# Performance work log

Measured on AMD Instinct MI355X. Metric: run time of the kernel, lower is better.

## Reference

```python
import math
import jax, jax.numpy as jnp
import numpy as np

B, N, C = 2, 2048, 256
TOPK_COARSE = 128
TOPK_FINE = 16
LOCAL_RAD = math.radians(15.0)
TEMP = 0.07
NEG = -1e9


def setup_inputs() -> dict:
    key = jax.random.key(0)
    ks = jax.random.split(key, 8)
    feat_a = jax.random.normal(ks[0], (B, N, C), jnp.float32)
    feat_b = jax.random.normal(ks[1], (B, N, C), jnp.float32)
    da = jax.random.normal(ks[2], (B, N, 3), jnp.float32)
    db = jax.random.normal(ks[3], (B, N, 3), jnp.float32)
    dirs_a = da / jnp.linalg.norm(da, axis=-1, keepdims=True)
    dirs_b = db / jnp.linalg.norm(db, axis=-1, keepdims=True)
    s = 1.0 / np.sqrt(C).astype(np.float32)
    Wq = jax.random.normal(ks[4], (C, C), jnp.float32) * s
    bq = jax.random.normal(ks[5], (C,), jnp.float32) * 0.01
    Wk = jax.random.normal(ks[6], (C, C), jnp.float32) * s
    bk = jax.random.normal(ks[7], (C,), jnp.float32) * 0.01
    return {"feat_a": feat_a, "feat_b": feat_b, "dirs_a": dirs_a, "dirs_b": dirs_b,
            "Wq": Wq, "bq": bq, "Wk": Wk, "bk": bk}


def reference(feat_a, feat_b, dirs_a, dirs_b, Wq, bq, Wk, bk):
    b, n, c = feat_a.shape
    q = feat_a @ Wq.T + bq                         # [B,N,C]
    k = feat_b @ Wk.T + bk                         # [B,N,C]

    # coarse stage: top-k over full similarity (math identical to chunked topk)
    sim = jnp.einsum('bnc,bmc->bnm', q, k)         # [B,N,N]
    _, coarse_idx = jax.lax.top_k(sim, TOPK_COARSE)  # [B,N,Kc]

    bi = jnp.arange(b)[:, None, None]
    k_cand = k[bi, coarse_idx]                     # [B,N,Kc,C]
    db_cand = dirs_b[bi, coarse_idx]               # [B,N,Kc,3]

    # angular locality mask (non-differentiable path)
    cosang = jnp.clip(jnp.sum(dirs_a[:, :, None, :] * db_cand, -1), -1.0, 1.0)
    ang = jnp.arccos(jax.lax.stop_gradient(cosang))
    local_mask = ang <= LOCAL_RAD                  # [B,N,Kc]
    # per-row fallback to all-ones (subsumes the chunk-level torch.any check)
    valid = local_mask.any(-1, keepdims=True)
    eff = jnp.where(valid, local_mask, True)

    logits_full = jnp.einsum('bnc,bnkc->bnk', q, k_cand) / TEMP
    logits_full = jnp.where(eff, logits_full, NEG)

    # fine stage: keep top TOPK_FINE candidates per row
    topk_vals, topk_pos = jax.lax.top_k(logits_full, TOPK_FINE)  # [B,N,Kf]
    idx = jnp.take_along_axis(coarse_idx, topk_pos, -1)
    eff_f = jnp.take_along_axis(eff, topk_pos, -1)
    fallback = eff_f.any(-1, keepdims=True)
    eff_f = jnp.where(fallback, eff_f, True)
    logits = jnp.where(eff_f, topk_vals, NEG)

    probs = jax.nn.softmax(logits, axis=-1) * eff_f.astype(logits.dtype)

    # scatter sparse support into dense P (indices distinct per row -> set is safe)
    ri = jnp.arange(n)[None, :, None]
    P = jnp.zeros((b, n, n), feat_a.dtype).at[bi, ri, idx].set(probs)
    P = P / (P.sum(-1, keepdims=True) + 1e-8)
    return P
```

## Files before the change

### kernel.cpp

```cpp
#include <hip/hip_runtime.h>
#include <hip/hip_bf16.h>
#include <math.h>

#define NN_ 2048
#define CC_ 256
#define KC_ 128
#define KF_ 16
#define EQCAP 64

typedef __attribute__((ext_vector_type(8))) short short8;
typedef __attribute__((ext_vector_type(4))) float f32x4;

__device__ __forceinline__ unsigned int mono_u(float f) {
  unsigned int u = __float_as_uint(f);
  return (u & 0x80000000u) ? ~u : (u | 0x80000000u);
}
__device__ __forceinline__ float inv_mono(unsigned int m) {
  unsigned int u = (m & 0x80000000u) ? (m ^ 0x80000000u) : ~m;
  return __uint_as_float(u);
}

__device__ __forceinline__ void gload_lds16(const void* g, void* l) {
  __builtin_amdgcn_global_load_lds(
      (const __attribute__((address_space(1))) void*)g,
      (__attribute__((address_space(3))) void*)l, 16, 0, 0);
}

__device__ __forceinline__ unsigned short bf16_bits(float v) {
  __hip_bfloat16 h = __float2bfloat16(v);
  return *(unsigned short*)&h;
}
__device__ __forceinline__ float bf16_val(unsigned short u) {
  __hip_bfloat16 h = *(__hip_bfloat16*)&u;
  return __bfloat162float(h);
}

__global__ __launch_bounds__(256) void proj_mfma_kernel(
    const float* __restrict__ fa, const float* __restrict__ fb,
    const float* __restrict__ Wq, const float* __restrict__ bq,
    const float* __restrict__ Wk, const float* __restrict__ bk,
    __hip_bfloat16* __restrict__ qh, __hip_bfloat16* __restrict__ ql,
    __hip_bfloat16* __restrict__ kh, __hip_bfloat16* __restrict__ kl)
{
  __shared__ short Ah[64 * 32], Al[64 * 32], Bh[64 * 32], Bl[64 * 32];
  const int m0 = blockIdx.y * 64;
  const int z = m0 >> 12;
  const int mloc = m0 & 4095;
  const float* A = z ? fb : fa;
  const float* W = z ? Wk : Wq;
  const float* bias = z ? bk : bq;
  __hip_bfloat16* oh = z ? kh : qh;
  __hip_bfloat16* ol = z ? kl : ql;
  const int n0 = blockIdx.x * 64;
  const int tid = threadIdx.x;
  const int lane = tid & 63, wave = tid >> 6;
  const int wm = (wave & 1) << 5, wn = (wave >> 1) << 5;
  const int fm = lane & 15, quad = lane >> 4;

  const int r = tid >> 3;
  const int r2 = r + 32;
  const int c4 = (tid & 7) << 2;
  const int ck = c4 >> 3;
  const int soff = c4 & 7;
  const int iA0 = (((r << 2) + (ck ^ ((r >> 1) & 3))) << 3) + soff;
  const int iA1 = (((r2 << 2) + (ck ^ ((r2 >> 1) & 3))) << 3) + soff;

  f32x4 acc[2][2];
#pragma unroll
  for (int i = 0; i < 2; ++i)
#pragma unroll
    for (int j = 0; j < 2; ++j) acc[i][j] = (f32x4){0.f, 0.f, 0.f, 0.f};

  for (int kb = 0; kb < CC_; kb += 32) {
    float4 va0 = *(const float4*)(A + (long)(mloc + r) * CC_ + kb + c4);
    float4 va1 = *(const float4*)(A + (long)(mloc + r2) * CC_ + kb + c4);
    float4 vb0 = *(const float4*)(W + (long)(n0 + r) * CC_ + kb + c4);
    float4 vb1 = *(const float4*)(W + (long)(n0 + r2) * CC_ + kb + c4);
    __syncthreads();
    {
      const float* pv;
      float4 vv;
      vv = va0; pv = (const float*)&vv;
      uint2 hu, lu;
      unsigned short h0 = bf16_bits(pv[0]), h1 = bf16_bits(pv[1]),
                     h2 = bf16_bits(pv[2]), h3 = bf16_bits(pv[3]);
      hu.x = (unsigned)h0 | ((unsigned)h1 << 16);
      hu.y = (unsigned)h2 | ((unsigned)h3 << 16);
      lu.x = (unsigned)bf16_bits(pv[0] - bf16_val(h0)) |
             ((unsigned)bf16_bits(pv[1] - bf16_val(h1)) << 16);
      lu.y = (unsigned)bf16_bits(pv[2] - bf16_val(h2)) |
             ((unsigned)bf16_bits(pv[3] - bf16_val(h3)) << 16);
      *(uint2*)&Ah[iA0] = hu; *(uint2*)&Al[iA0] = lu;
      vv = va1; pv = (const float*)&vv;
      h0 = bf16_bits(pv[0]); h1 = bf16_bits(pv[1]);
      h2 = bf16_bits(pv[2]); h3 = bf16_bits(pv[3]);
      hu.x = (unsigned)h0 | ((unsigned)h1 << 16);
      hu.y = (unsigned)h2 | ((unsigned)h3 << 16);
      lu.x = (unsigned)bf16_bits(pv[0] - bf16_val(h0)) |
             ((unsigned)bf16_bits(pv[1] - bf16_val(h1)) << 16);
      lu.y = (unsigned)bf16_bits(pv[2] - bf16_val(h2)) |
             ((unsigned)bf16_bits(pv[3] - bf16_val(h3)) << 16);
      *(uint2*)&Ah[iA1] = hu; *(uint2*)&Al[iA1] = lu;
      vv = vb0; pv = (const float*)&vv;
      h0 = bf16_bits(pv[0]); h1 = bf16_bits(pv[1]);
      h2 = bf16_bits(pv[2]); h3 = bf16_bits(pv[3]);
      hu.x = (unsigned)h0 | ((unsigned)h1 << 16);
      hu.y = (unsigned)h2 | ((unsigned)h3 << 16);
      lu.x = (unsigned)bf16_bits(pv[0] - bf16_val(h0)) |
             ((unsigned)bf16_bits(pv[1] - bf16_val(h1)) << 16);
      lu.y = (unsigned)bf16_bits(pv[2] - bf16_val(h2)) |
             ((unsigned)bf16_bits(pv[3] - bf16_val(h3)) << 16);
      *(uint2*)&Bh[iA0] = hu; *(uint2*)&Bl[iA0] = lu;
      vv = vb1; pv = (const float*)&vv;
      h0 = bf16_bits(pv[0]); h1 = bf16_bits(pv[1]);
      h2 = bf16_bits(pv[2]); h3 = bf16_bits(pv[3]);
      hu.x = (unsigned)h0 | ((unsigned)h1 << 16);
      hu.y = (unsigned)h2 | ((unsigned)h3 << 16);
      lu.x = (unsigned)bf16_bits(pv[0] - bf16_val(h0)) |
             ((unsigned)bf16_bits(pv[1] - bf16_val(h1)) << 16);
      lu.y = (unsigned)bf16_bits(pv[2] - bf16_val(h2)) |
             ((unsigned)bf16_bits(pv[3] - bf16_val(h3)) << 16);
      *(uint2*)&Bh[iA1] = hu; *(uint2*)&Bl[iA1] = lu;
    }
    __syncthreads();
    short8 afh[2], afl[2], bfh[2], bfl[2];
#pragma unroll
    for (int t = 0; t < 2; ++t) {
      int m = wm + (t << 4) + fm;
      int sa = ((m << 2) + (quad ^ ((m >> 1) & 3))) << 3;
      afh[t] = *(const short8*)&Ah[sa];
      afl[t] = *(const short8*)&Al[sa];
      int n = wn + (t << 4) + fm;
      int sb = ((n << 2) + (quad ^ ((n >> 1) & 3))) << 3;
      bfh[t] = *(const short8*)&Bh[sb];
      bfl[t] = *(const short8*)&Bl[sb];
    }
#pragma unroll
    for (int mi = 0; mi < 2; ++mi)
#pragma unroll
      for (int ni = 0; ni < 2; ++ni) {
        acc[mi][ni] = __builtin_amdgcn_mfma_f32_16x16x32_bf16(
            afh[mi], bfh[ni], acc[mi][ni], 0, 0, 0);
        acc[mi][ni] = __builtin_amdgcn_mfma_f32_16x16x32_bf16(
            afh[mi], bfl[ni], acc[mi][ni], 0, 0, 0);
        acc[mi][ni] = __builtin_amdgcn_mfma_f32_16x16x32_bf16(
            afl[mi], bfh[ni], acc[mi][ni], 0, 0, 0);
      }
  }

#pragma unroll
  for (int mi = 0; mi < 2; ++mi)
#pragma unroll
    for (int ni = 0; ni < 2; ++ni) {
      int nn = n0 + wn + (ni << 4) + fm;
      float bval = bias[nn];
      int mrow = mloc + wm + (mi << 4) + (quad << 2);
#pragma unroll
      for (int reg = 0; reg < 4; ++reg) {
        float v = acc[mi][ni][reg] + bval;
        __hip_bfloat16 h = __float2bfloat16(v);
        long idx = (long)(mrow + reg) * CC_ + nn;
        oh[idx] = h;
        ol[idx] = __float2bfloat16(v - __bfloat162float(h));
      }
    }
}

__global__ __launch_bounds__(256) void sim_mfma_kernel(
    const __hip_bfloat16* __restrict__ qh, const __hip_bfloat16* __restrict__ ql,
    const __hip_bfloat16* __restrict__ kh, const __hip_bfloat16* __restrict__ kl,
    float* __restrict__ sim)
{
  __shared__ short Ah[128 * 32], Al[128 * 32], Bh[128 * 32], Bl[128 * 32];
  const int z = blockIdx.z;
  const long off = (long)z * NN_ * CC_;
  const int m0 = blockIdx.y * 128, n0 = blockIdx.x * 128;
  const int tid = threadIdx.x;
  const int lane = tid & 63, wave = tid >> 6;
  const int wm = (wave & 1) << 6, wn = (wave >> 1) << 6;
  const int fm = lane & 15, quad = lane >> 4;

  const int r0 = tid >> 2, r1 = r0 + 64;
  const int c0 = (((tid & 3) ^ ((r0 >> 1) & 3)) << 3);
  const int c1 = (((tid & 3) ^ ((r1 >> 1) & 3)) << 3);
  const long lo0 = (long)tid * 8, lo1 = ((long)tid + 256) * 8;
  const long gA0 = (long)(m0 + r0) * CC_ + c0 + off;
  const long gA1 = (long)(m0 + r1) * CC_ + c1 + off;
  const long gB0 = (long)(n0 + r0) * CC_ + c0 + off;
  const long gB1 = (long)(n0 + r1) * CC_ + c1 + off;

  f32x4 acc[4][4];
#pragma unroll
  for (int i = 0; i < 4; ++i)
#pragma unroll
    for (int j = 0; j < 4; ++j) acc[i][j] = (f32x4){0.f, 0.f, 0.f, 0.f};

  for (int kb = 0; kb < CC_; kb += 32) {
    gload_lds16(qh + gA0 + kb, Ah + lo0);
    gload_lds16(qh + gA1 + kb, Ah + lo1);
    gload_lds16(ql + gA0 + kb, Al + lo0);
    gload_lds16(ql + gA1 + kb, Al + lo1);
    gload_lds16(kh + gB0 + kb, Bh + lo0);
    gload_lds16(kh + gB1 + kb, Bh + lo1);
    gload_lds16(kl + gB0 + kb, Bl + lo0);
    gload_lds16(kl + gB1 + kb, Bl + lo1);
    __syncthreads();
    short8 afh[4], afl[4], bfh[4], bfl[4];
#pragma unroll
    for (int t = 0; t < 4; ++t) {
      int m = wm + (t << 4) + fm;
      int sa = ((m << 2) + (quad ^ ((m >> 1) & 3))) << 3;
      afh[t] = *(const short8*)&Ah[sa];
      afl[t] = *(const short8*)&Al[sa];
      int n = wn + (t << 4) + fm;
      int sb = ((n << 2) + (quad ^ ((n >> 1) & 3))) << 3;
      bfh[t] = *(const short8*)&Bh[sb];
      bfl[t] = *(const short8*)&Bl[sb];
    }
#pragma unroll
    for (int mi = 0; mi < 4; ++mi)
#pragma unroll
      for (int ni = 0; ni < 4; ++ni) {
        acc[mi][ni] = __builtin_amdgcn_mfma_f32_16x16x32_bf16(
            afh[mi], bfh[ni], acc[mi][ni], 0, 0, 0);
        acc[mi][ni] = __builtin_amdgcn_mfma_f32_16x16x32_bf16(
            afh[mi], bfl[ni], acc[mi][ni], 0, 0, 0);
        acc[mi][ni] = __builtin_amdgcn_mfma_f32_16x16x32_bf16(
            afl[mi], bfh[ni], acc[mi][ni], 0, 0, 0);
      }
    __syncthreads();
  }

  float* Cp = sim + (long)z * NN_ * NN_;
#pragma unroll
  for (int mi = 0; mi < 4; ++mi) {
#pragma unroll
    for (int ni = 0; ni < 4; ++ni) {
      int m = m0 + wm + (mi << 4) + (quad << 2);
      int n = n0 + wn + (ni << 4) + fm;
      float* p = Cp + (long)m * NN_ + n;
      p[0] = acc[mi][ni][0];
      p[NN_] = acc[mi][ni][1];
      p[2 * NN_] = acc[mi][ni][2];
      p[3 * NN_] = acc[mi][ni][3];
    }
  }
}

__global__ __launch_bounds__(256) void select_scatter_kernel(
    const float* __restrict__ sim, const float* __restrict__ dirs_a,
    const float* __restrict__ dirs_b, float* __restrict__ P)
{
  const int wave = threadIdx.x >> 6;
  const int lane = threadIdx.x & 63;
  const int row = (blockIdx.x << 2) | wave;
  const int b = row >> 11;
  const float* srow = sim + (long)row * NN_;
  float* prow = P + (long)row * NN_;

  __shared__ unsigned int ckey_s[4][KC_];
  __shared__ int cidx_s[4][KC_];
  __shared__ int eq_s[4][EQCAP];
  __shared__ float outp_s[4][KF_];
  __shared__ int outj_s[4][KF_];
  __shared__ float rowbuf_s[4][1024];
  __shared__ int cnt_s[4][2];

  unsigned int* ckey = ckey_s[wave];
  int* cidx = cidx_s[wave];
  int* eqb = eq_s[wave];
  float* outp = outp_s[wave];
  int* outj = outj_s[wave];
  float* rowbuf = rowbuf_s[wave];
  int* cnt = cnt_s[wave];

  unsigned int key[32];
#pragma unroll
  for (int c = 0; c < 8; ++c) {
    float4 v = *(const float4*)(srow + (c << 8) + (lane << 2));
    key[(c << 2) + 0] = mono_u(v.x);
    key[(c << 2) + 1] = mono_u(v.y);
    key[(c << 2) + 2] = mono_u(v.z);
    key[(c << 2) + 3] = mono_u(v.w);
  }

  unsigned int lo = 0u, hi = 0xFFFFFFFFu;
  while (hi - lo > 1u) {
    unsigned int mid = lo + ((hi - lo) >> 1);
    int c = 0;
#pragma unroll
    for (int i = 0; i < 32; ++i)
      c += __popcll(__ballot(key[i] >= mid));
    if (c >= KC_) lo = mid; else hi = mid;
  }
  const unsigned int T = lo;
  int cgt = 0;
#pragma unroll
  for (int i = 0; i < 32; ++i)
    cgt += __popcll(__ballot(key[i] > T));
  const int count_gt = cgt;
  const int need_eq = KC_ - cgt;

  if (lane == 0) { cnt[0] = 0; cnt[1] = 0; }
#pragma unroll
  for (int i = 0; i < 32; ++i) {
    unsigned int u = key[i];
    int col = ((i >> 2) << 8) + (lane << 2) + (i & 3);
    if (u > T) {
      int p = atomicAdd(&cnt[0], 1);
      ckey[p] = u;
      cidx[p] = col;
    } else if (u == T) {
      int p = atomicAdd(&cnt[1], 1);
      if (p < EQCAP) eqb[p] = col;
    }
  }
  int neq = cnt[1];
  if (lane == 0) {
    if (neq <= EQCAP) {
      for (int r = 0; r < need_eq; ++r) {
        int best = 0x7FFFFFFF, bi = 0;
        for (int t2 = 0; t2 < neq; ++t2)
          if (eqb[t2] < best) { best = eqb[t2]; bi = t2; }
        eqb[bi] = 0x7FFFFFFF;
        ckey[count_gt + r] = T;
        cidx[count_gt + r] = best;
      }
    } else {
      int r2 = 0;
      for (int j = 0; j < NN_ && r2 < need_eq; ++j)
        if (mono_u(srow[j]) == T) {
          ckey[count_gt + r2] = T;
          cidx[count_gt + r2] = j;
          ++r2;
        }
    }
  }

  const long dbase = (long)row * 3;
  const float dax = dirs_a[dbase + 0], day = dirs_a[dbase + 1],
              daz = dirs_a[dbase + 2];
  int j0 = cidx[lane], j1 = cidx[lane + 64];
  float va0 = inv_mono(ckey[lane]), va1 = inv_mono(ckey[lane + 64]);
  const float* db0 = dirs_b + ((long)(b << 11) + j0) * 3;
  float ca0 = dax * db0[0] + day * db0[1] + daz * db0[2];
  const float* db1 = dirs_b + ((long)(b << 11) + j1) * 3;
  float ca1 = dax * db1[0] + day * db1[1] + daz * db1[2];
  bool lm0 = ca0 >= 0.96592582628906831f;
  bool lm1 = ca1 >= 0.96592582628906831f;
  int ecnt = __popcll(__ballot(lm0)) + __popcll(__ballot(lm1));
  const bool all = (ecnt == 0);
  float v0 = (all || lm0) ? va0 : -INFINITY;
  float v1 = (all || lm1) ? va1 : -INFINITY;
  const int elig = all ? KC_ : ecnt;
  const int nk = elig < KF_ ? elig : KF_;

  for (int r = 0; r < nk; ++r) {
    float bvv; int bj, bs;
    if (v1 > v0 || (v1 == v0 && j1 < j0)) { bvv = v1; bj = j1; bs = lane + 64; }
    else { bvv = v0; bj = j0; bs = lane; }
#pragma unroll
    for (int off = 32; off > 0; off >>= 1) {
      float ov = __shfl_down(bvv, off);
      int oj = __shfl_down(bj, off);
      int os = __shfl_down(bs, off);
      if (ov > bvv || (ov == bvv && oj < bj)) { bvv = ov; bj = oj; bs = os; }
    }
    bvv = __shfl(bvv, 0); bj = __shfl(bj, 0); bs = __shfl(bs, 0);
    if (lane == 0) { outj[r] = bj; outp[r] = bvv; }
    if (bs == lane) v0 = -INFINITY;
    if (bs == lane + 64) v1 = -INFINITY;
  }

  const float invT = 1.0f / 0.07f;
  float mxl = outp[0] * invT;
  float e = 0.f;
  int myj = 0;
  if (lane < nk) {
    e = __expf(outp[lane] * invT - mxl);
    myj = outj[lane];
  }
  float ssum = e;
#pragma unroll
  for (int off = 32; off > 0; off >>= 1) ssum += __shfl_xor(ssum, off);
  float pr = e / ssum;
  float s2 = pr;
#pragma unroll
  for (int off = 32; off > 0; off >>= 1) s2 += __shfl_xor(s2, off);
  const float outv = pr * (1.0f / (s2 + 1e-8f));

#pragma unroll
  for (int h = 0; h < 2; ++h) {
    float4 zf; zf.x = zf.y = zf.z = zf.w = 0.f;
#pragma unroll
    for (int q = 0; q < 4; ++q)
      *(float4*)&rowbuf[(q << 8) + (lane << 2)] = zf;
    if (lane < nk && (myj >> 10) == h) rowbuf[myj & 1023] = outv;
#pragma unroll
    for (int q = 0; q < 4; ++q) {
      float4 v = *(const float4*)&rowbuf[(q << 8) + (lane << 2)];
      *(float4*)(prow + (h << 10) + (q << 8) + (lane << 2)) = v;
    }
  }
}

extern "C" void kernel_launch(void* const* d_in, const int* in_sizes, int n_in,
                              void* d_out, int out_size, void* d_ws, size_t ws_size,
                              hipStream_t stream) {
  (void)in_sizes; (void)n_in; (void)out_size; (void)ws_size;
  const float* feat_a = (const float*)d_in[0];
  const float* feat_b = (const float*)d_in[1];
  const float* dirs_a = (const float*)d_in[2];
  const float* dirs_b = (const float*)d_in[3];
  const float* Wq = (const float*)d_in[4];
  const float* bq = (const float*)d_in[5];
  const float* Wk = (const float*)d_in[6];
  const float* bk = (const float*)d_in[7];
  float* P = (float*)d_out;

  __hip_bfloat16* qh = (__hip_bfloat16*)d_ws;
  __hip_bfloat16* ql = qh + (long)2 * NN_ * CC_;
  __hip_bfloat16* kh = ql + (long)2 * NN_ * CC_;
  __hip_bfloat16* kl = kh + (long)2 * NN_ * CC_;
  float* sim = (float*)(kl + (long)2 * NN_ * CC_);

  proj_mfma_kernel<<<dim3(CC_ / 64, (4 * NN_) / 64), 256, 0, stream>>>(
      feat_a, feat_b, Wq, bq, Wk, bk, qh, ql, kh, kl);

  sim_mfma_kernel<<<dim3(NN_ / 128, NN_ / 128, 2), 256, 0, stream>>>(
      qh, ql, kh, kl, sim);

  select_scatter_kernel<<<dim3((2 * NN_) / 4), 256, 0, stream>>>(
      sim, dirs_a, dirs_b, P);
}
```

Measured before the change: 153.5 us.

## Replace bitwise binary-search top-k threshold with 11-bit histogram radix select

The top-128 threshold search ran a 32-step binary search, each step doing 32 ballots over the row. It is replaced by a single 2048-bin histogram over the top 11 key bits, built with packed 16-bit LDS atomics, followed by a wave suffix scan to find the boundary bin. The elements still needed from that boundary bin are then picked one at a time by wave-wide argmax reductions. The histogram buffer shares LDS with the row buffer. The cost is that the boundary-bin selection loop can run up to 128 reduction rounds when many values fall in the same bin.

```diff
diff --git a/kernel.cpp b/kernel.cpp
--- a/kernel.cpp
+++ b/kernel.cpp
@@ -6,7 +6,6 @@
 #define CC_ 256
 #define KC_ 128
 #define KF_ 16
-#define EQCAP 64
 
 typedef __attribute__((ext_vector_type(8))) short short8;
 typedef __attribute__((ext_vector_type(4))) float f32x4;
@@ -258,21 +257,19 @@
   const float* srow = sim + (long)row * NN_;
   float* prow = P + (long)row * NN_;
 
+  __shared__ unsigned int histbuf_s[4][1024];
   __shared__ unsigned int ckey_s[4][KC_];
   __shared__ int cidx_s[4][KC_];
-  __shared__ int eq_s[4][EQCAP];
   __shared__ float outp_s[4][KF_];
   __shared__ int outj_s[4][KF_];
-  __shared__ float rowbuf_s[4][1024];
-  __shared__ int cnt_s[4][2];
-
+  __shared__ int cnt_s[4];
+
+  unsigned int* histw = histbuf_s[wave];
+  float* rowbuf = (float*)histbuf_s[wave];
   unsigned int* ckey = ckey_s[wave];
   int* cidx = cidx_s[wave];
-  int* eqb = eq_s[wave];
   float* outp = outp_s[wave];
   int* outj = outj_s[wave];
-  float* rowbuf = rowbuf_s[wave];
-  int* cnt = cnt_s[wave];
 
   unsigned int key[32];
 #pragma unroll
@@ -284,57 +281,86 @@
     key[(c << 2) + 3] = mono_u(v.w);
   }
 
-  unsigned int lo = 0u, hi = 0xFFFFFFFFu;
-  while (hi - lo > 1u) {
-    unsigned int mid = lo + ((hi - lo) >> 1);
-    int c = 0;
-#pragma unroll
-    for (int i = 0; i < 32; ++i)
-      c += __popcll(__ballot(key[i] >= mid));
-    if (c >= KC_) lo = mid; else hi = mid;
-  }
-  const unsigned int T = lo;
-  int cgt = 0;
-#pragma unroll
-  for (int i = 0; i < 32; ++i)
-    cgt += __popcll(__ballot(key[i] > T));
-  const int count_gt = cgt;
-  const int need_eq = KC_ - cgt;
-
-  if (lane == 0) { cnt[0] = 0; cnt[1] = 0; }
+  {
+    uint4 z4; z4.x = z4.y = z4.z = z4.w = 0u;
+#pragma unroll
+    for (int t = 0; t < 4; ++t)
+      *(uint4*)&histw[(lane << 4) + (t << 2)] = z4;
+  }
 #pragma unroll
   for (int i = 0; i < 32; ++i) {
-    unsigned int u = key[i];
-    int col = ((i >> 2) << 8) + (lane << 2) + (i & 3);
-    if (u > T) {
-      int p = atomicAdd(&cnt[0], 1);
-      ckey[p] = u;
+    unsigned int bin = key[i] >> 21;
+    atomicAdd(&histw[bin >> 1], 1u << ((bin & 1) << 4));
+  }
+  unsigned int c16[32];
+#pragma unroll
+  for (int t = 0; t < 4; ++t) {
+    uint4 w = *(const uint4*)&histw[(lane << 4) + (t << 2)];
+    c16[(t << 3) + 0] = w.x & 0xFFFFu; c16[(t << 3) + 1] = w.x >> 16;
+    c16[(t << 3) + 2] = w.y & 0xFFFFu; c16[(t << 3) + 3] = w.y >> 16;
+    c16[(t << 3) + 4] = w.z & 0xFFFFu; c16[(t << 3) + 5] = w.z >> 16;
+    c16[(t << 3) + 6] = w.w & 0xFFFFu; c16[(t << 3) + 7] = w.w >> 16;
+  }
+  unsigned int tot = 0;
+#pragma unroll
+  for (int i = 0; i < 32; ++i) tot += c16[i];
+  unsigned int incl = tot;
+#pragma unroll
+  for (int off = 1; off < 64; off <<= 1) {
+    unsigned int y = __shfl_down(incl, off);
+    incl += (lane + off < 64) ? y : 0u;
+  }
+  const unsigned int sufx = incl - tot;
+  int li = -1;
+  unsigned int run = 0, cge_l = 0, cB_l = 0;
+  for (int i = 31; i >= 0; --i) {
+    run += c16[i];
+    if (run + sufx >= (unsigned)KC_) {
+      li = i; cge_l = run + sufx; cB_l = c16[i];
+      break;
+    }
+  }
+  unsigned long long mb = __ballot(li >= 0);
+  const int src = 63 - __clzll(mb);
+  const unsigned int B = (unsigned)__shfl((lane << 5) + li, src);
+  const unsigned int cge = __shfl(cge_l, src);
+  const unsigned int cB = __shfl(cB_l, src);
+  const int ngt = (int)(cge - cB);
+  const int need_rem = KC_ - ngt;
+
+  if (lane == 0) cnt_s[wave] = 0;
+#pragma unroll
+  for (int i = 0; i < 32; ++i) {
+    if ((key[i] >> 21) > B) {
+      int col = ((i >> 2) << 8) + (lane << 2) + (i & 3);
+      int p = atomicAdd(&cnt_s[wave], 1);
+      ckey[p] = key[i];
       cidx[p] = col;
-    } else if (u == T) {
-      int p = atomicAdd(&cnt[1], 1);
-      if (p < EQCAP) eqb[p] = col;
-    }
-  }
-  int neq = cnt[1];
-  if (lane == 0) {
-    if (neq <= EQCAP) {
-      for (int r = 0; r < need_eq; ++r) {
-        int best = 0x7FFFFFFF, bi = 0;
-        for (int t2 = 0; t2 < neq; ++t2)
-          if (eqb[t2] < best) { best = eqb[t2]; bi = t2; }
-        eqb[bi] = 0x7FFFFFFF;
-        ckey[count_gt + r] = T;
-        cidx[count_gt + r] = best;
+    }
+  }
+  unsigned int taken = 0u;
+  for (int r = 0; r < need_rem; ++r) {
+    unsigned int bk = 0u; int bi = 0x7FFFFFFF, bslot = -1;
+#pragma unroll
+    for (int i = 0; i < 32; ++i) {
+      if (!((taken >> i) & 1u) && (key[i] >> 21) == B) {
+        int col = ((i >> 2) << 8) + (lane << 2) + (i & 3);
+        if (key[i] > bk || (key[i] == bk && col < bi)) {
+          bk = key[i]; bi = col; bslot = i;
+        }
       }
-    } else {
-      int r2 = 0;
-      for (int j = 0; j < NN_ && r2 < need_eq; ++j)
-        if (mono_u(srow[j]) == T) {
-          ckey[count_gt + r2] = T;
-          cidx[count_gt + r2] = j;
-          ++r2;
-        }
-    }
+    }
+    int bl = lane;
+#pragma unroll
+    for (int off = 32; off > 0; off >>= 1) {
+      unsigned int ok = __shfl_down(bk, off);
+      int oi = __shfl_down(bi, off);
+      int ol = __shfl_down(bl, off);
+      if (ok > bk || (ok == bk && oi < bi)) { bk = ok; bi = oi; bl = ol; }
+    }
+    bk = __shfl(bk, 0); bi = __shfl(bi, 0); bl = __shfl(bl, 0);
+    if (lane == 0) { ckey[ngt + r] = bk; cidx[ngt + r] = bi; }
+    if (lane == bl && bslot >= 0) taken |= 1u << bslot;
   }
 
   const long dbase = (long)row * 3;
```

After: 308.3 us. +100.9%, slower.
